# Performance work log

Hardware: AMD Instinct MI355X
Metric: run time of the kernel (lower is better)

The kernel has to match this reference:

```python
import jax, jax.numpy as jnp
import numpy as np

DIM = 384
HEADS = 12
HEAD_DIM = DIM // HEADS
WIN = (2, 7, 7)
NW_TOK = WIN[0] * WIN[1] * WIN[2]  # 98
SCALE = HEAD_DIM ** -0.5


def _relative_position_index():
    d = np.arange(WIN[0]); h = np.arange(WIN[1]); w = np.arange(WIN[2])
    coords = np.stack(np.meshgrid(d, h, w, indexing='ij'))  # [3,D,H,W]
    cf = coords.reshape(3, -1)  # [3, NW_TOK]
    rel = cf[:, :, None] - cf[:, None, :]  # [3, N, N]
    rel = rel.transpose(1, 2, 0).astype(np.int64)
    rel[:, :, 0] += WIN[0] - 1
    rel[:, :, 1] += WIN[1] - 1
    rel[:, :, 2] += WIN[2] - 1
    rel[:, :, 0] *= (2 * WIN[1] - 1) * (2 * WIN[2] - 1)
    rel[:, :, 1] *= 2 * WIN[2] - 1
    return rel.sum(-1)  # [NW_TOK, NW_TOK]


def setup_inputs() -> dict:
    key = jax.random.key(0)
    ks = jax.random.split(key, 6)
    B_, N = 1024, NW_TOK + 1
    nW = 64
    table_len = (2 * WIN[0] - 1) * (2 * WIN[1] - 1) * (2 * WIN[2] - 1)  # 507
    x = jax.random.normal(ks[0], (B_, N, DIM), dtype=jnp.float32)
    mask = jax.random.normal(ks[1], (nW, NW_TOK, NW_TOK), dtype=jnp.float32)
    W_qkv = jax.random.normal(ks[2], (DIM, 3 * DIM), dtype=jnp.float32) * 0.02
    rpb_table = jax.random.normal(ks[3], (table_len, HEADS), dtype=jnp.float32) * 0.02
    W_proj = jax.random.normal(ks[4], (DIM, DIM), dtype=jnp.float32) * 0.02
    b_proj = jnp.zeros((DIM,), dtype=jnp.float32)
    rpi = jnp.asarray(_relative_position_index(), dtype=jnp.int32)
    return {"x": x, "mask": mask, "W_qkv": W_qkv, "rpb_table": rpb_table,
            "W_proj": W_proj, "b_proj": b_proj, "rpi": rpi}


def reference(x, mask, W_qkv, rpb_table, W_proj, b_proj, rpi):
    B_, N, C = x.shape
    qkv = (x @ W_qkv).reshape(B_, N, 3, HEADS, HEAD_DIM)
    q, k, v = qkv[:, :, 0], qkv[:, :, 1], qkv[:, :, 2]  # [B_, N, H, hd]
    attn = jnp.einsum('bnhd,bmhd->bhnm', q * SCALE, k)  # [B_, H, N, N]
    # gathered relative position bias over non-class tokens, zero-padded for class token
    bias = rpb_table[rpi.reshape(-1)].reshape(NW_TOK, NW_TOK, HEADS).transpose(2, 0, 1)
    bias_full = jnp.pad(bias, ((0, 0), (1, 0), (1, 0)))  # [H, N, N]
    attn = attn + bias_full[None]
    nW = mask.shape[0]
    mask_full = jnp.pad(mask, ((0, 0), (1, 0), (1, 0)))  # [nW, N, N]
    attn = attn.reshape(B_ // nW, nW, HEADS, N, N) + mask_full[None, :, None]
    attn = attn.reshape(B_, HEADS, N, N)
    attn = jax.nn.softmax(attn, axis=-1)
    out = jnp.einsum('bhnm,bmhd->bnhd', attn, v).reshape(B_, N, C)
    out = out @ W_proj + b_proj
    return out[:, 1:], out[:, :1]
```

## Files before the change

kernel.cpp:

```cpp
#include <hip/hip_runtime.h>
#include <hip/hip_bf16.h>
#include <cstddef>
#include <cstdint>


using bf16 = __hip_bfloat16;
typedef short v8s __attribute__((ext_vector_type(8)));
typedef short v4s __attribute__((ext_vector_type(4)));
typedef float v4f __attribute__((ext_vector_type(4)));

static constexpr int    NTOK   = 99;
static constexpr int    CDIM   = 384;
static constexpr int    NHEAD  = 12;
static constexpr int    NROWS  = 101376;
static constexpr size_t PLANE  = (size_t)NROWS * 32;
static constexpr float  SCALEF = 0.17677669529663687f;

__device__ __forceinline__ v4f mfma16x16x32(v8s a, v8s b, v4f c) {
  return __builtin_amdgcn_mfma_f32_16x16x32_bf16(a, b, c, 0, 0, 0);
}
__device__ __forceinline__ short f2bf(float f) {
  bf16 h = __float2bfloat16(f);
  return *reinterpret_cast<short*>(&h);
}
__device__ __forceinline__ float bf2f(short s) {
  bf16 h = *reinterpret_cast<bf16*>(&s);
  return __bfloat162float(h);
}

#if defined(__has_builtin)
#if __has_builtin(__builtin_amdgcn_global_load_lds)
#define HAS_GLL 1
#endif
#endif
#ifndef HAS_GLL
#define HAS_GLL 0
#endif

__device__ __forceinline__ void gload_lds16(const bf16* gsrc, bf16* ldst, int lane) {
#if HAS_GLL
  __builtin_amdgcn_global_load_lds(
      (const __attribute__((address_space(1))) void*)gsrc,
      (__attribute__((address_space(3))) void*)ldst, 16, 0, 0);
#else
  *(v8s*)(ldst + lane * 8) = *(const v8s*)gsrc;
#endif
}

static constexpr size_t WT_QKV_OFF = 0;
static constexpr size_t WT_P_OFF   = 884736;
static constexpr size_t BIAS_OFF   = 884736 + 294912;
static constexpr size_t COMMON_END = 1650096;
static constexpr size_t O_WS_OFF   = COMMON_END;
static constexpr size_t WS_MID     = O_WS_OFF + (size_t)NROWS * 384 * 2;
static constexpr size_t BMF_OFF    = COMMON_END;
static constexpr size_t BMF_BYTES  = (size_t)64 * NHEAD * 7 * 7 * 64 * 4 * 2;
static constexpr size_t QKV_OFF    = BMF_OFF + BMF_BYTES;
static constexpr size_t WS_FULL    = QKV_OFF + (size_t)NROWS * 1152 * 2;

static constexpr int PREP_BASE = 1152 * 384 + 384 * 384 + NHEAD * 99 * 99;
static constexpr int PREP_BMF2 = 64 * 112 * 112;

__global__ void prep_kernel(const float* __restrict__ Wqkv, const float* __restrict__ Wproj,
                            const float* __restrict__ rpb,  const int* __restrict__ rpi,
                            const float* __restrict__ mask,
                            bf16* __restrict__ WtQKV, bf16* __restrict__ WtP,
                            float* __restrict__ BIAS, bf16* __restrict__ BMF, int do_bmf)
{
  int idx = blockIdx.x * 256 + threadIdx.x;
  if (idx < 1152 * 384) {
    int c = idx / 384, k = idx - c * 384;
    WtQKV[idx] = __float2bfloat16(Wqkv[k * 1152 + c]);
  } else if (idx < 1152 * 384 + 384 * 384) {
    int j = idx - 1152 * 384;
    int c = j / 384, k = j - c * 384;
    WtP[j] = __float2bfloat16(Wproj[k * 384 + c]);
  } else if (idx < PREP_BASE) {
    int j = idx - (1152 * 384 + 384 * 384);
    int h = j / (99 * 99), r = j % (99 * 99);
    int nn = r / 99, mm = r % 99;
    float v = 0.f;
    if (nn > 0 && mm > 0) v = rpb[rpi[(nn - 1) * 98 + (mm - 1)] * NHEAD + h];
    BIAS[j] = v;
  } else if (do_bmf && idx < PREP_BASE + PREP_BMF2) {
    int j2  = idx - PREP_BASE;
    int col = j2 % 112;
    int r2  = j2 / 112;
    int row = r2 % 112;
    int wi  = r2 / 112;
    int w = row >> 4, g = (row >> 2) & 3, jj = row & 3;
    int t = col >> 4, li = col & 15, lane = g * 16 + li;
    bool in = (row >= 1 && row <= 98 && col >= 1 && col <= 98);
    int tix = 0; float mval = 0.f;
    if (in) {
      tix  = rpi[(row - 1) * 98 + (col - 1)];
      mval = mask[((size_t)wi * 98 + (row - 1)) * 98 + (col - 1)];
    }
    size_t base = (((size_t)wi * NHEAD * 7 + w) * 7 + t) * 256 + lane * 4 + jj;
    #pragma unroll
    for (int h = 0; h < NHEAD; ++h) {
      float v = in ? (rpb[tix * NHEAD + h] + mval) : 0.f;
      BMF[base + (size_t)h * 12544] = __float2bfloat16(v);
    }
  }
}

static constexpr int GQB_OFF  = 0;
static constexpr int GQA_OFF  = 24576;
static constexpr int GQ_LDS2  = GQA_OFF + 128 * 72 * 2;
static constexpr int CSTG_LD  = 104;

__global__ __launch_bounds__(512)
void k_qkv(const float* __restrict__ x, const bf16* __restrict__ WtQKV,
           bf16* __restrict__ qkv2)
{
  __shared__ __align__(16) char smem[GQ_LDS2];
  bf16* B_lds = (bf16*)(smem + GQB_OFF);
  bf16* A_lds = (bf16*)(smem + GQA_OFF);
  bf16* C_stg = (bf16*)(smem);

  const int tid  = threadIdx.x;
  const int wave = tid >> 6;
  const int wm   = wave >> 2;
  const int wn   = wave & 3;
  const int lane = tid & 63;
  const int g    = lane >> 4;
  const int li   = lane & 15;
  const int tile = (blockIdx.x & 7) * 594 + (blockIdx.x >> 3);
  const int R0   = (tile / 6) * 128;
  const int CN   = (tile % 6) * 192;

  const int arr = tid >> 3, ak8 = tid & 7;

  v4f acc[4][3];
  #pragma unroll
  for (int mi = 0; mi < 4; ++mi)
    #pragma unroll
    for (int ni = 0; ni < 3; ++ni) acc[mi][ni] = (v4f){0.f, 0.f, 0.f, 0.f};

  v4f areg[2][2];
  auto load_areg = [&](int kc) {
    const int k0 = kc * 64;
    #pragma unroll
    for (int p = 0; p < 2; ++p) {
      const float* src = x + (size_t)(R0 + arr + p * 64) * 384 + k0 + ak8 * 8;
      areg[p][0] = *(const v4f*)(src);
      areg[p][1] = *(const v4f*)(src + 4);
    }
  };
  auto write_alds = [&]() {
    #pragma unroll
    for (int p = 0; p < 2; ++p) {
      v8s f;
      #pragma unroll
      for (int j = 0; j < 4; ++j) { f[j] = f2bf(areg[p][0][j]); f[j + 4] = f2bf(areg[p][1][j]); }
      *(v8s*)(A_lds + (arr + p * 64) * 72 + ak8 * 8) = f;
    }
  };

  load_areg(0);

  for (int kc = 0; kc < 6; ++kc) {
    const int k0 = kc * 64;
    write_alds();
    #pragma unroll
    for (int p = 0; p < 3; ++p) {
      int q   = wave * 3 + p;
      int row = q * 8 + (lane >> 3);
      int c   = (lane & 7) ^ (row & 7);
      const bf16* gsrc = WtQKV + (size_t)(CN + row) * 384 + k0 + c * 8;
      gload_lds16(gsrc, B_lds + q * 512, lane);
    }
    if (kc < 5) load_areg(kc + 1);
    __syncthreads();
    #pragma unroll
    for (int ks = 0; ks < 2; ++ks) {
      v8s af[4], bfr[3];
      #pragma unroll
      for (int mi = 0; mi < 4; ++mi)
        af[mi] = *(const v8s*)(A_lds + (wm * 64 + mi * 16 + li) * 72 + ks * 32 + g * 8);
      #pragma unroll
      for (int ni = 0; ni < 3; ++ni) {
        int brow = wn * 48 + ni * 16 + li;
        int sc   = (g + 4 * ks) ^ (brow & 7);
        bfr[ni]  = *(const v8s*)(B_lds + brow * 64 + sc * 8);
      }
      #pragma unroll
      for (int mi = 0; mi < 4; ++mi)
        #pragma unroll
        for (int ni = 0; ni < 3; ++ni)
          acc[mi][ni] = mfma16x16x32(af[mi], bfr[ni], acc[mi][ni]);
    }
    __syncthreads();
  }

  const float scale = (CN < 384) ? SCALEF : 1.f;
  const int r_ep = tid >> 2, d8 = tid & 3;
  #pragma unroll
  for (int half = 0; half < 2; ++half) {
    __syncthreads();
    if ((wn >> 1) == half) {
      #pragma unroll
      for (int mi = 0; mi < 4; ++mi)
        #pragma unroll
        for (int ni = 0; ni < 3; ++ni)
          #pragma unroll
          for (int j = 0; j < 4; ++j)
            C_stg[(wm * 64 + mi * 16 + g * 4 + j) * CSTG_LD + (wn & 1) * 48 + ni * 16 + li] =
                __float2bfloat16(acc[mi][ni][j] * scale);
    }
    __syncthreads();
    #pragma unroll
    for (int cidx = 0; cidx < 3; ++cidx) {
      int c_global = CN + half * 96 + cidx * 32;
      int seg = c_global / 384, hh = (c_global % 384) >> 5;
      bf16* plane = qkv2 + (size_t)(hh * 3 + seg) * PLANE;
      v8s val = *(const v8s*)(C_stg + r_ep * CSTG_LD + cidx * 32 + d8 * 8);
      *(v8s*)(plane + (size_t)(R0 + r_ep) * 32 + d8 * 8) = val;
    }
  }
}

static constexpr int A_VT_LD = 136;
static constexpr int A_P_LD  = 136;
static constexpr int A_OFF_V = 0;
static constexpr int A_OFF_P = A_OFF_V + 32 * A_VT_LD * 2;
static constexpr int A_LDS   = A_OFF_P + 112 * A_P_LD * 2;

__global__ __launch_bounds__(448)
void k_attn(const bf16* __restrict__ BMF, bf16* __restrict__ qkv2)
{
  __shared__ __align__(16) char smem[A_LDS];
  bf16* vT_lds = (bf16*)(smem + A_OFF_V);
  bf16* P_lds  = (bf16*)(smem + A_OFF_P);

  const int b    = blockIdx.x;
  const int h0   = blockIdx.y * 3;
  const int tid  = threadIdx.x;
  const int wave = tid >> 6;
  const int lane = tid & 63;
  const int g    = lane >> 4;
  const int li   = lane & 15;
  const int wi   = b & 63;

  for (int z = tid; z < 32 * 29; z += 448)
    vT_lds[(z / 29) * A_VT_LD + 99 + (z % 29)] = __float2bfloat16(0.f);
  for (int z = tid; z < 112 * 29; z += 448)
    P_lds[(z / 29) * A_P_LD + 99 + (z % 29)] = __float2bfloat16(0.f);

  const int r = tid >> 2, l4 = tid & 3;
  const size_t voff = ((size_t)b * NTOK + ((r > 98) ? 98 : r)) * 32 + l4 * 8;

  const int qrow = (16 * wave + li > 98) ? 98 : 16 * wave + li;
  const size_t qoff = ((size_t)b * NTOK + qrow) * 32 + g * 8;
  size_t koff[7];
  #pragma unroll
  for (int t = 0; t < 7; ++t) {
    int krow = 16 * t + li; if (krow > 98) krow = 98;
    koff[t] = ((size_t)b * NTOK + krow) * 32 + g * 8;
  }

  {
    v8s pv = *(const v8s*)(qkv2 + (size_t)(h0 * 3 + 2) * PLANE + voff);
    if (r < NTOK) {
      #pragma unroll
      for (int e = 0; e < 8; ++e)
        *(short*)(vT_lds + (l4 * 8 + e) * A_VT_LD + r) = pv[e];
    }
  }
  __syncthreads();

  v4f oaccs[3][2];

  #pragma unroll
  for (int hi = 0; hi < 3; ++hi) {
    const int h = h0 + hi;
    v8s nv;
    if (hi < 2) nv = *(const v8s*)(qkv2 + (size_t)(h * 3 + 5) * PLANE + voff);

    const bf16* kp = qkv2 + (size_t)(h * 3 + 1) * PLANE;
    v8s kf[7];
    #pragma unroll
    for (int t = 0; t < 7; ++t) kf[t] = *(const v8s*)(kp + koff[t]);
    v8s qf = *(const v8s*)(qkv2 + (size_t)(h * 3 + 0) * PLANE + qoff);

    const bf16* bmb = BMF + ((size_t)((wi * NHEAD + h) * 7 + wave) * 7) * 256;
    v4s bmr[7];
    #pragma unroll
    for (int t = 0; t < 7; ++t)
      bmr[t] = *(const v4s*)(bmb + t * 256 + lane * 4);

    v4f sacc[7];
    #pragma unroll
    for (int t = 0; t < 7; ++t) {
      v4f z = (v4f){0.f, 0.f, 0.f, 0.f};
      sacc[t] = mfma16x16x32(qf, kf[t], z);
    }
    #pragma unroll
    for (int t = 0; t < 7; ++t) {
      int col = 16 * t + li;
      #pragma unroll
      for (int j = 0; j < 4; ++j) {
        float s = sacc[t][j];
        if (col >= NTOK) s = -1e30f;
        else             s += bf2f(bmr[t][j]);
        sacc[t][j] = s;
      }
    }
    float linv[4];
    #pragma unroll
    for (int j = 0; j < 4; ++j) {
      float m = -1e30f;
      #pragma unroll
      for (int t = 0; t < 7; ++t) m = fmaxf(m, sacc[t][j]);
      m = fmaxf(m, __shfl_xor(m, 1));
      m = fmaxf(m, __shfl_xor(m, 2));
      m = fmaxf(m, __shfl_xor(m, 4));
      m = fmaxf(m, __shfl_xor(m, 8));
      float l = 0.f;
      #pragma unroll
      for (int t = 0; t < 7; ++t) {
        float p = __expf(sacc[t][j] - m);
        sacc[t][j] = p;
        l += p;
      }
      l += __shfl_xor(l, 1);
      l += __shfl_xor(l, 2);
      l += __shfl_xor(l, 4);
      l += __shfl_xor(l, 8);
      linv[j] = 1.f / l;
      int row = 16 * wave + g * 4 + j;
      #pragma unroll
      for (int t = 0; t < 7; ++t) {
        int col = 16 * t + li;
        if (col < NTOK) P_lds[row * A_P_LD + col] = __float2bfloat16(sacc[t][j]);
      }
    }
    v4f oacc[2];
    oacc[0] = (v4f){0.f, 0.f, 0.f, 0.f};
    oacc[1] = (v4f){0.f, 0.f, 0.f, 0.f};
    #pragma unroll
    for (int ks = 0; ks < 4; ++ks) {
      v8s ap = *(const v8s*)(P_lds + (16 * wave + li) * A_P_LD + ks * 32 + g * 8);
      #pragma unroll
      for (int t = 0; t < 2; ++t) {
        v8s bv = *(const v8s*)(vT_lds + (16 * t + li) * A_VT_LD + ks * 32 + g * 8);
        oacc[t] = mfma16x16x32(ap, bv, oacc[t]);
      }
    }
    #pragma unroll
    for (int t = 0; t < 2; ++t)
      #pragma unroll
      for (int j = 0; j < 4; ++j)
        oaccs[hi][t][j] = oacc[t][j] * linv[j];

    __syncthreads();
    if (hi < 2) {
      if (r < NTOK) {
        #pragma unroll
        for (int e = 0; e < 8; ++e)
          *(short*)(vT_lds + (l4 * 8 + e) * A_VT_LD + r) = nv[e];
      }
      __syncthreads();
    }
  }

  #pragma unroll
  for (int hi = 0; hi < 3; ++hi) {
    bf16* oplane = qkv2 + (size_t)((h0 + hi) * 3) * PLANE;
    #pragma unroll
    for (int t = 0; t < 2; ++t)
      #pragma unroll
      for (int j = 0; j < 4; ++j) {
        int row = 16 * wave + g * 4 + j;
        if (row < NTOK)
          oplane[((size_t)b * NTOK + row) * 32 + 16 * t + li] =
              __float2bfloat16(oaccs[hi][t][j]);
      }
  }
}

static constexpr int K2_LD   = 72;
static constexpr int K2_OFFW = 0;
static constexpr int K2_OFFO = 192 * K2_LD * 2;
static constexpr int K2_LDS  = K2_OFFO + 128 * K2_LD * 2;

__global__ __launch_bounds__(512)
void k2_proj(const bf16* __restrict__ O_src, const int hm,
             const bf16* __restrict__ WtP, const float* __restrict__ bproj,
             float* __restrict__ out)
{
  __shared__ __align__(16) char smem[K2_LDS];
  bf16* W_lds = (bf16*)(smem + K2_OFFW);
  bf16* O_lds = (bf16*)(smem + K2_OFFO);

  const int tid  = threadIdx.x;
  const int wave = tid >> 6;
  const int wm   = wave >> 2;
  const int wn   = wave & 3;
  const int lane = tid & 63;
  const int g    = lane >> 4;
  const int li   = lane & 15;
  const int tile = (blockIdx.x & 7) * 198 + (blockIdx.x >> 3);
  const int R0   = (tile >> 1) * 128;
  const int CN   = (tile & 1) * 192;

  v4f acc[4][3];
  #pragma unroll
  for (int mi = 0; mi < 4; ++mi)
    #pragma unroll
    for (int ni = 0; ni < 3; ++ni) acc[mi][ni] = (v4f){0.f, 0.f, 0.f, 0.f};

  for (int kc = 0; kc < 6; ++kc) {
    const int k0 = kc * 64;
    #pragma unroll
    for (int p = 0; p < 3; ++p) {
      int it = tid + p * 512, rr = it >> 3, k8 = it & 7;
      *(v8s*)(W_lds + rr * K2_LD + k8 * 8) =
          *(const v8s*)(WtP + (size_t)(CN + rr) * CDIM + k0 + k8 * 8);
    }
    #pragma unroll
    for (int p = 0; p < 2; ++p) {
      int it = tid + p * 512, rr = it >> 3, k8 = it & 7;
      const bf16* src;
      if (hm) {
        int c = k0 + k8 * 8, hh = c >> 5, d = c & 31;
        src = O_src + (size_t)(hh * 3) * PLANE + (size_t)(R0 + rr) * 32 + d;
      } else {
        src = O_src + (size_t)(R0 + rr) * 384 + k0 + k8 * 8;
      }
      *(v8s*)(O_lds + rr * K2_LD + k8 * 8) = *(const v8s*)src;
    }
    __syncthreads();
    #pragma unroll
    for (int ks = 0; ks < 2; ++ks) {
      v8s af[4], bfr[3];
      #pragma unroll
      for (int mi = 0; mi < 4; ++mi)
        af[mi] = *(const v8s*)(O_lds + (wm * 64 + mi * 16 + li) * K2_LD + ks * 32 + g * 8);
      #pragma unroll
      for (int ni = 0; ni < 3; ++ni)
        bfr[ni] = *(const v8s*)(W_lds + (wn * 48 + ni * 16 + li) * K2_LD + ks * 32 + g * 8);
      #pragma unroll
      for (int mi = 0; mi < 4; ++mi)
        #pragma unroll
        for (int ni = 0; ni < 3; ++ni)
          acc[mi][ni] = mfma16x16x32(af[mi], bfr[ni], acc[mi][ni]);
    }
    __syncthreads();
  }

  const size_t OUT2 = (size_t)1024 * 98 * CDIM;
  #pragma unroll
  for (int mi = 0; mi < 4; ++mi)
    #pragma unroll
    for (int ni = 0; ni < 3; ++ni) {
      int col = CN + wn * 48 + ni * 16 + li;
      float bb = bproj[col];
      #pragma unroll
      for (int j = 0; j < 4; ++j) {
        int rr = R0 + wm * 64 + mi * 16 + g * 4 + j;
        int b = rr / 99, n = rr - b * 99;
        float v = acc[mi][ni][j] + bb;
        if (n == 0) out[OUT2 + (size_t)b * CDIM + col] = v;
        else        out[((size_t)b * 98 + (n - 1)) * CDIM + col] = v;
      }
    }
}

static constexpr int QK_LD = 40;
static constexpr int VT_LD = 136;
static constexpr int P_LD  = 136;
static constexpr int WS_LD = 104;
static constexpr int K1_OFF_Q = 0;
static constexpr int K1_OFF_K = K1_OFF_Q + 112 * QK_LD * 2;
static constexpr int K1_OFF_V = K1_OFF_K + 112 * QK_LD * 2;
static constexpr int K1_OFF_P = K1_OFF_V + 32  * VT_LD * 2;
static constexpr int K1_OFF_W = K1_OFF_P + 112 * P_LD  * 2;
static constexpr int K1_LDS   = K1_OFF_W + 96 * WS_LD * 2;

__global__ __launch_bounds__(512)
void k1_attn(const float* __restrict__ x, const float* __restrict__ mask,
             const float* __restrict__ BIAS, const bf16* __restrict__ WtQKV,
             bf16* __restrict__ O_ws)
{
  __shared__ __align__(16) char smem[K1_LDS];
  bf16* q_lds  = (bf16*)(smem + K1_OFF_Q);
  bf16* k_lds  = (bf16*)(smem + K1_OFF_K);
  bf16* vT_lds = (bf16*)(smem + K1_OFF_V);
  bf16* P_lds  = (bf16*)(smem + K1_OFF_P);
  bf16* w_lds  = (bf16*)(smem + K1_OFF_W);

  const int b    = blockIdx.x;
  const int tid  = threadIdx.x;
  const int wave = tid >> 6;
  const int lane = tid & 63;
  const int g    = lane >> 4;
  const int li   = lane & 15;
  const int wi   = b & 63;

  v8s afr[12];
  if (wave < 7) {
    int arow = 16 * wave + li; if (arow > 98) arow = 98;
    const float* xb = x + ((size_t)b * NTOK + arow) * CDIM + g * 8;
    #pragma unroll
    for (int s = 0; s < 12; ++s) {
      v4f x0 = *(const v4f*)(xb + s * 32);
      v4f x1 = *(const v4f*)(xb + s * 32 + 4);
      v8s f;
      #pragma unroll
      for (int j = 0; j < 4; ++j) { f[j] = f2bf(x0[j]); f[j + 4] = f2bf(x1[j]); }
      afr[s] = f;
    }
  }

  for (int h = 0; h < NHEAD; ++h) {
    v4f qacc[6];
    #pragma unroll
    for (int t = 0; t < 6; ++t) qacc[t] = (v4f){0.f, 0.f, 0.f, 0.f};
    #pragma unroll
    for (int c4 = 0; c4 < 4; ++c4) {
      for (int idx = tid; idx < 96 * 12; idx += 512) {
        int rr = idx / 12, ch = idx - rr * 12;
        int cg = (rr < 32) ? (h * 32 + rr)
               : (rr < 64) ? (CDIM + h * 32 + rr - 32)
                           : (2 * CDIM + h * 32 + rr - 64);
        *(v8s*)(w_lds + rr * WS_LD + ch * 8) =
            *(const v8s*)(WtQKV + (size_t)cg * CDIM + c4 * 96 + ch * 8);
      }
      __syncthreads();
      if (wave < 7) {
        #pragma unroll
        for (int ss = 0; ss < 3; ++ss) {
          const int s = c4 * 3 + ss;
          #pragma unroll
          for (int t = 0; t < 6; ++t) {
            v8s bw = *(const v8s*)(w_lds + (16 * t + li) * WS_LD + ss * 32 + g * 8);
            qacc[t] = mfma16x16x32(afr[s], bw, qacc[t]);
          }
        }
      }
      __syncthreads();
    }
    if (wave < 7) {
      #pragma unroll
      for (int t = 0; t < 6; ++t) {
        #pragma unroll
        for (int j = 0; j < 4; ++j) {
          int row = 16 * wave + g * 4 + j;
          int col = 16 * (t & 1) + li;
          float v = qacc[t][j];
          if (t < 2)      q_lds[row * QK_LD + col] = __float2bfloat16(v * SCALEF);
          else if (t < 4) k_lds[row * QK_LD + col] = __float2bfloat16(v);
          else            vT_lds[col * VT_LD + row] = __float2bfloat16(v);
        }
      }
    }
    vT_lds[(tid >> 4) * VT_LD + 112 + (tid & 15)] = __float2bfloat16(0.f);
    __syncthreads();

    if (wave < 7) {
      v8s aq = *(const v8s*)(q_lds + (16 * wave + li) * QK_LD + g * 8);
      v4f sacc[7];
      #pragma unroll
      for (int t = 0; t < 7; ++t) {
        v8s bk = *(const v8s*)(k_lds + (16 * t + li) * QK_LD + g * 8);
        v4f z = (v4f){0.f, 0.f, 0.f, 0.f};
        sacc[t] = mfma16x16x32(aq, bk, z);
      }
      #pragma unroll
      for (int t = 0; t < 7; ++t) {
        int col = 16 * t + li;
        #pragma unroll
        for (int j = 0; j < 4; ++j) {
          int row = 16 * wave + g * 4 + j;
          float s = sacc[t][j];
          if (col >= NTOK) s = -1e30f;
          else if (row < NTOK) {
            s += BIAS[(h * NTOK + row) * NTOK + col];
            if (row > 0 && col > 0)
              s += mask[((size_t)wi * 98 + (row - 1)) * 98 + (col - 1)];
          }
          sacc[t][j] = s;
        }
      }
      float linv[4];
      #pragma unroll
      for (int j = 0; j < 4; ++j) {
        float m = -1e30f;
        #pragma unroll
        for (int t = 0; t < 7; ++t) m = fmaxf(m, sacc[t][j]);
        m = fmaxf(m, __shfl_xor(m, 1));
        m = fmaxf(m, __shfl_xor(m, 2));
        m = fmaxf(m, __shfl_xor(m, 4));
        m = fmaxf(m, __shfl_xor(m, 8));
        float l = 0.f;
        #pragma unroll
        for (int t = 0; t < 7; ++t) {
          float p = __expf(sacc[t][j] - m);
          sacc[t][j] = p;
          l += p;
        }
        l += __shfl_xor(l, 1);
        l += __shfl_xor(l, 2);
        l += __shfl_xor(l, 4);
        l += __shfl_xor(l, 8);
        linv[j] = 1.f / l;
        int row = 16 * wave + g * 4 + j;
        #pragma unroll
        for (int t = 0; t < 7; ++t)
          P_lds[row * P_LD + 16 * t + li] = __float2bfloat16(sacc[t][j]);
        P_lds[row * P_LD + 112 + li] = __float2bfloat16(0.f);
      }
      v4f oacc[2];
      oacc[0] = (v4f){0.f, 0.f, 0.f, 0.f};
      oacc[1] = (v4f){0.f, 0.f, 0.f, 0.f};
      #pragma unroll
      for (int ks = 0; ks < 4; ++ks) {
        v8s ap = *(const v8s*)(P_lds + (16 * wave + li) * P_LD + ks * 32 + g * 8);
        #pragma unroll
        for (int t = 0; t < 2; ++t) {
          v8s bv = *(const v8s*)(vT_lds + (16 * t + li) * VT_LD + ks * 32 + g * 8);
          oacc[t] = mfma16x16x32(ap, bv, oacc[t]);
        }
      }
      #pragma unroll
      for (int t = 0; t < 2; ++t) {
        #pragma unroll
        for (int j = 0; j < 4; ++j) {
          int row = 16 * wave + g * 4 + j;
          if (row < NTOK)
            O_ws[((size_t)b * 99 + row) * CDIM + h * 32 + 16 * t + li] =
                __float2bfloat16(oacc[t][j] * linv[j]);
        }
      }
    }
    __syncthreads();
  }
}

static constexpr int M_O_LD = 392;
static constexpr int M_OFF_O = 0;
static constexpr int M_OFF_Q = M_OFF_O + 99  * M_O_LD * 2;
static constexpr int M_OFF_K = M_OFF_Q + 112 * QK_LD * 2;
static constexpr int M_OFF_V = M_OFF_K + 112 * QK_LD * 2;
static constexpr int M_OFF_P = M_OFF_V + 32  * VT_LD * 2;
static constexpr int M_OFF_W = M_OFF_P + 112 * P_LD  * 2;
static constexpr int M_LDS   = M_OFF_W + 96 * WS_LD * 2;

__global__ __launch_bounds__(512)
void fused_mono(const float* __restrict__ x, const float* __restrict__ mask,
                const float* __restrict__ bproj, const float* __restrict__ BIAS,
                const bf16* __restrict__ WtQKV, const bf16* __restrict__ WtP,
                float* __restrict__ out)
{
  __shared__ __align__(16) char smem[M_LDS];
  bf16* O_lds  = (bf16*)(smem + M_OFF_O);
  bf16* q_lds  = (bf16*)(smem + M_OFF_Q);
  bf16* k_lds  = (bf16*)(smem + M_OFF_K);
  bf16* vT_lds = (bf16*)(smem + M_OFF_V);
  bf16* P_lds  = (bf16*)(smem + M_OFF_P);
  bf16* w_lds  = (bf16*)(smem + M_OFF_W);

  const int b    = blockIdx.x;
  const int tid  = threadIdx.x;
  const int wave = tid >> 6;
  const int lane = tid & 63;
  const int g    = lane >> 4;
  const int li   = lane & 15;
  const int wi   = b & 63;

  v8s afr[12];
  if (wave < 7) {
    int arow = 16 * wave + li; if (arow > 98) arow = 98;
    const float* xb = x + ((size_t)b * NTOK + arow) * CDIM + g * 8;
    #pragma unroll
    for (int s = 0; s < 12; ++s) {
      v4f x0 = *(const v4f*)(xb + s * 32);
      v4f x1 = *(const v4f*)(xb + s * 32 + 4);
      v8s f;
      #pragma unroll
      for (int j = 0; j < 4; ++j) { f[j] = f2bf(x0[j]); f[j + 4] = f2bf(x1[j]); }
      afr[s] = f;
    }
  }

  for (int h = 0; h < NHEAD; ++h) {
    v4f qacc[6];
    #pragma unroll
    for (int t = 0; t < 6; ++t) qacc[t] = (v4f){0.f, 0.f, 0.f, 0.f};
    #pragma unroll
    for (int c4 = 0; c4 < 4; ++c4) {
      for (int idx = tid; idx < 96 * 12; idx += 512) {
        int rr = idx / 12, ch = idx - rr * 12;
        int cg = (rr < 32) ? (h * 32 + rr)
               : (rr < 64) ? (CDIM + h * 32 + rr - 32)
                           : (2 * CDIM + h * 32 + rr - 64);
        *(v8s*)(w_lds + rr * WS_LD + ch * 8) =
            *(const v8s*)(WtQKV + (size_t)cg * CDIM + c4 * 96 + ch * 8);
      }
      __syncthreads();
      if (wave < 7) {
        #pragma unroll
        for (int ss = 0; ss < 3; ++ss) {
          const int s = c4 * 3 + ss;
          #pragma unroll
          for (int t = 0; t < 6; ++t) {
            v8s bw = *(const v8s*)(w_lds + (16 * t + li) * WS_LD + ss * 32 + g * 8);
            qacc[t] = mfma16x16x32(afr[s], bw, qacc[t]);
          }
        }
      }
      __syncthreads();
    }
    if (wave < 7) {
      #pragma unroll
      for (int t = 0; t < 6; ++t) {
        #pragma unroll
        for (int j = 0; j < 4; ++j) {
          int row = 16 * wave + g * 4 + j;
          int col = 16 * (t & 1) + li;
          float v = qacc[t][j];
          if (t < 2)      q_lds[row * QK_LD + col] = __float2bfloat16(v * SCALEF);
          else if (t < 4) k_lds[row * QK_LD + col] = __float2bfloat16(v);
          else            vT_lds[col * VT_LD + row] = __float2bfloat16(v);
        }
      }
    }
    vT_lds[(tid >> 4) * VT_LD + 112 + (tid & 15)] = __float2bfloat16(0.f);
    __syncthreads();

    if (wave < 7) {
      v8s aq = *(const v8s*)(q_lds + (16 * wave + li) * QK_LD + g * 8);
      v4f sacc[7];
      #pragma unroll
      for (int t = 0; t < 7; ++t) {
        v8s bk = *(const v8s*)(k_lds + (16 * t + li) * QK_LD + g * 8);
        v4f z = (v4f){0.f, 0.f, 0.f, 0.f};
        sacc[t] = mfma16x16x32(aq, bk, z);
      }
      #pragma unroll
      for (int t = 0; t < 7; ++t) {
        int col = 16 * t + li;
        #pragma unroll
        for (int j = 0; j < 4; ++j) {
          int row = 16 * wave + g * 4 + j;
          float s = sacc[t][j];
          if (col >= NTOK) s = -1e30f;
          else if (row < NTOK) {
            s += BIAS[(h * NTOK + row) * NTOK + col];
            if (row > 0 && col > 0)
              s += mask[((size_t)wi * 98 + (row - 1)) * 98 + (col - 1)];
          }
          sacc[t][j] = s;
        }
      }
      float linv[4];
      #pragma unroll
      for (int j = 0; j < 4; ++j) {
        float m = -1e30f;
        #pragma unroll
        for (int t = 0; t < 7; ++t) m = fmaxf(m, sacc[t][j]);
        m = fmaxf(m, __shfl_xor(m, 1));
        m = fmaxf(m, __shfl_xor(m, 2));
        m = fmaxf(m, __shfl_xor(m, 4));
        m = fmaxf(m, __shfl_xor(m, 8));
        float l = 0.f;
        #pragma unroll
        for (int t = 0; t < 7; ++t) {
          float p = __expf(sacc[t][j] - m);
          sacc[t][j] = p;
          l += p;
        }
        l += __shfl_xor(l, 1);
        l += __shfl_xor(l, 2);
        l += __shfl_xor(l, 4);
        l += __shfl_xor(l, 8);
        linv[j] = 1.f / l;
        int row = 16 * wave + g * 4 + j;
        #pragma unroll
        for (int t = 0; t < 7; ++t)
          P_lds[row * P_LD + 16 * t + li] = __float2bfloat16(sacc[t][j]);
        P_lds[row * P_LD + 112 + li] = __float2bfloat16(0.f);
      }
      v4f oacc[2];
      oacc[0] = (v4f){0.f, 0.f, 0.f, 0.f};
      oacc[1] = (v4f){0.f, 0.f, 0.f, 0.f};
      #pragma unroll
      for (int ks = 0; ks < 4; ++ks) {
        v8s ap = *(const v8s*)(P_lds + (16 * wave + li) * P_LD + ks * 32 + g * 8);
        #pragma unroll
        for (int t = 0; t < 2; ++t) {
          v8s bv = *(const v8s*)(vT_lds + (16 * t + li) * VT_LD + ks * 32 + g * 8);
          oacc[t] = mfma16x16x32(ap, bv, oacc[t]);
        }
      }
      #pragma unroll
      for (int t = 0; t < 2; ++t) {
        #pragma unroll
        for (int j = 0; j < 4; ++j) {
          int row = 16 * wave + g * 4 + j;
          if (row < NTOK)
            O_lds[row * M_O_LD + h * 32 + 16 * t + li] =
                __float2bfloat16(oacc[t][j] * linv[j]);
        }
      }
    }
    __syncthreads();
  }

  const size_t OUT2 = (size_t)1024 * 98 * CDIM;
  const int orow_clamped = (16 * wave + li > 98) ? 98 : 16 * wave + li;
  for (int cc = 0; cc < 4; ++cc) {
    v4f pacc[6];
    #pragma unroll
    for (int t = 0; t < 6; ++t) pacc[t] = (v4f){0.f, 0.f, 0.f, 0.f};
    for (int c4 = 0; c4 < 4; ++c4) {
      for (int idx = tid; idx < 96 * 12; idx += 512) {
        int rr = idx / 12, ch = idx - rr * 12;
        *(v8s*)(w_lds + rr * WS_LD + ch * 8) =
            *(const v8s*)(WtP + ((size_t)(cc * 96 + rr)) * CDIM + c4 * 96 + ch * 8);
      }
      __syncthreads();
      if (wave < 7) {
        #pragma unroll
        for (int ss = 0; ss < 3; ++ss) {
          const int s = c4 * 3 + ss;
          v8s ao = *(const v8s*)(O_lds + orow_clamped * M_O_LD + s * 32 + g * 8);
          #pragma unroll
          for (int t = 0; t < 6; ++t) {
            v8s bw = *(const v8s*)(w_lds + (16 * t + li) * WS_LD + ss * 32 + g * 8);
            pacc[t] = mfma16x16x32(ao, bw, pacc[t]);
          }
        }
      }
      __syncthreads();
    }
    if (wave < 7) {
      #pragma unroll
      for (int t = 0; t < 6; ++t) {
        #pragma unroll
        for (int j = 0; j < 4; ++j) {
          int row = 16 * wave + g * 4 + j;
          if (row < NTOK) {
            int col = cc * 96 + 16 * t + li;
            float v = pacc[t][j] + bproj[col];
            if (row == 0) out[OUT2 + (size_t)b * CDIM + col] = v;
            else          out[((size_t)b * 98 + (row - 1)) * CDIM + col] = v;
          }
        }
      }
    }
  }
}

extern "C" void kernel_launch(void* const* d_in, const int* in_sizes, int n_in,
                              void* d_out, int out_size, void* d_ws, size_t ws_size,
                              hipStream_t stream) {
  const float* x     = (const float*)d_in[0];
  const float* mask  = (const float*)d_in[1];
  const float* Wqkv  = (const float*)d_in[2];
  const float* rpb   = (const float*)d_in[3];
  const float* Wproj = (const float*)d_in[4];
  const float* bproj = (const float*)d_in[5];
  const int*   rpi   = (const int*)d_in[6];

  bf16*  WtQKV = (bf16*)((char*)d_ws + WT_QKV_OFF);
  bf16*  WtP   = (bf16*)((char*)d_ws + WT_P_OFF);
  float* BIAS  = (float*)((char*)d_ws + BIAS_OFF);
  bf16*  BMF   = (bf16*)((char*)d_ws + BMF_OFF);

  const bool full = (ws_size >= WS_FULL);
  const int prep_items = full ? (PREP_BASE + PREP_BMF2) : PREP_BASE;
  prep_kernel<<<(prep_items + 255) / 256, 256, 0, stream>>>(
      Wqkv, Wproj, rpb, rpi, mask, WtQKV, WtP, BIAS, BMF, full ? 1 : 0);

  if (full) {
    bf16* qkv2 = (bf16*)((char*)d_ws + QKV_OFF);
    k_qkv<<<792 * 6, 512, 0, stream>>>(x, WtQKV, qkv2);
    k_attn<<<dim3(1024, 4), 448, 0, stream>>>(BMF, qkv2);
    k2_proj<<<792 * 2, 512, 0, stream>>>(qkv2, 1, WtP, bproj, (float*)d_out);
  } else if (ws_size >= WS_MID) {
    bf16* O_ws = (bf16*)((char*)d_ws + O_WS_OFF);
    k1_attn<<<1024, 512, 0, stream>>>(x, mask, BIAS, WtQKV, O_ws);
    k2_proj<<<792 * 2, 512, 0, stream>>>(O_ws, 0, WtP, bproj, (float*)d_out);
  } else {
    fused_mono<<<1024, 512, 0, stream>>>(x, mask, bproj, BIAS, WtQKV, WtP,
                                         (float*)d_out);
  }
}
```

Measured before the change: 434.1 us.

## Pre-convert x to bf16 and double-buffer QKV/proj GEMMs with direct LDS loads

Adds a pass in the prep kernel that converts x to bf16 into a new workspace buffer. New k_qkv2 and k2_proj2 kernels stage A and B tiles with global_load_lds into double-buffered, XOR-swizzled LDS and use vmcnt waits, so loads overlap the MFMA work. The goal is to hide global-load latency, avoid LDS bank conflicts and drop the fp32-to-bf16 conversion from the GEMM inner loop. In exchange it costs extra workspace plus an additional read and write pass over x, and the new path is taken only when the workspace is large enough.

```diff
diff --git a/kernel.cpp b/kernel.cpp
--- a/kernel.cpp
+++ b/kernel.cpp
@@ -57,15 +57,19 @@
 static constexpr size_t BMF_BYTES  = (size_t)64 * NHEAD * 7 * 7 * 64 * 4 * 2;
 static constexpr size_t QKV_OFF    = BMF_OFF + BMF_BYTES;
 static constexpr size_t WS_FULL    = QKV_OFF + (size_t)NROWS * 1152 * 2;
+static constexpr size_t XB_OFF     = WS_FULL;
+static constexpr size_t WS_FULL2   = XB_OFF + (size_t)NROWS * 384 * 2;
 
 static constexpr int PREP_BASE = 1152 * 384 + 384 * 384 + NHEAD * 99 * 99;
 static constexpr int PREP_BMF2 = 64 * 112 * 112;
+static constexpr int PREP_XB   = NROWS * 384 / 8;
 
 __global__ void prep_kernel(const float* __restrict__ Wqkv, const float* __restrict__ Wproj,
                             const float* __restrict__ rpb,  const int* __restrict__ rpi,
-                            const float* __restrict__ mask,
+                            const float* __restrict__ mask, const float* __restrict__ x,
                             bf16* __restrict__ WtQKV, bf16* __restrict__ WtP,
-                            float* __restrict__ BIAS, bf16* __restrict__ BMF, int do_bmf)
+                            float* __restrict__ BIAS, bf16* __restrict__ BMF,
+                            bf16* __restrict__ xb, int do_bmf, int do_xb)
 {
   int idx = blockIdx.x * 256 + threadIdx.x;
   if (idx < 1152 * 384) {
@@ -102,21 +106,28 @@
       float v = in ? (rpb[tix * NHEAD + h] + mval) : 0.f;
       BMF[base + (size_t)h * 12544] = __float2bfloat16(v);
     }
-  }
-}
-
-static constexpr int GQB_OFF  = 0;
-static constexpr int GQA_OFF  = 24576;
-static constexpr int GQ_LDS2  = GQA_OFF + 128 * 72 * 2;
-static constexpr int CSTG_LD  = 104;
+  } else if (do_xb && idx >= PREP_BASE + PREP_BMF2 &&
+             idx < PREP_BASE + PREP_BMF2 + PREP_XB) {
+    int j3 = idx - (PREP_BASE + PREP_BMF2);
+    size_t off = (size_t)j3 * 8;
+    v4f x0 = *(const v4f*)(x + off);
+    v4f x1 = *(const v4f*)(x + off + 4);
+    v8s f;
+    #pragma unroll
+    for (int j = 0; j < 4; ++j) { f[j] = f2bf(x0[j]); f[j + 4] = f2bf(x1[j]); }
+    *(v8s*)(xb + off) = f;
+  }
+}
+
+static constexpr int Q2_BUF  = 40960;
+static constexpr int Q2_AOFF = 24576;
+static constexpr int CSTG_LD = 104;
 
 __global__ __launch_bounds__(512)
-void k_qkv(const float* __restrict__ x, const bf16* __restrict__ WtQKV,
-           bf16* __restrict__ qkv2)
+void k_qkv2(const bf16* __restrict__ xb, const bf16* __restrict__ WtQKV,
+            bf16* __restrict__ qkv2)
 {
-  __shared__ __align__(16) char smem[GQ_LDS2];
-  bf16* B_lds = (bf16*)(smem + GQB_OFF);
-  bf16* A_lds = (bf16*)(smem + GQA_OFF);
+  __shared__ __align__(16) char smem[2 * Q2_BUF];
   bf16* C_stg = (bf16*)(smem);
 
   const int tid  = threadIdx.x;
@@ -130,6 +141,120 @@
   const int R0   = (tile / 6) * 128;
   const int CN   = (tile % 6) * 192;
 
+  v4f acc[4][3];
+  #pragma unroll
+  for (int mi = 0; mi < 4; ++mi)
+    #pragma unroll
+    for (int ni = 0; ni < 3; ++ni) acc[mi][ni] = (v4f){0.f, 0.f, 0.f, 0.f};
+
+  auto stage = [&](int kc, int buf) {
+    const int k0 = kc * 64;
+    bf16* Bl = (bf16*)(smem + buf * Q2_BUF);
+    bf16* Al = (bf16*)(smem + buf * Q2_BUF + Q2_AOFF);
+    #pragma unroll
+    for (int p = 0; p < 3; ++p) {
+      int q = wave * 3 + p;
+      int row = q * 8 + (lane >> 3);
+      int c = (lane & 7) ^ (row & 7);
+      gload_lds16(WtQKV + (size_t)(CN + row) * 384 + k0 + c * 8, Bl + q * 512, lane);
+    }
+    #pragma unroll
+    for (int p = 0; p < 2; ++p) {
+      int q = wave * 2 + p;
+      int row = q * 8 + (lane >> 3);
+      int c = (lane & 7) ^ (row & 7);
+      gload_lds16(xb + (size_t)(R0 + row) * 384 + k0 + c * 8, Al + q * 512, lane);
+    }
+  };
+
+  stage(0, 0);
+  for (int kc = 0; kc < 6; ++kc) {
+    if (kc < 5) {
+      stage(kc + 1, (kc + 1) & 1);
+      asm volatile("s_waitcnt vmcnt(5)" ::: "memory");
+    } else {
+      asm volatile("s_waitcnt vmcnt(0)" ::: "memory");
+    }
+    __builtin_amdgcn_s_barrier();
+    __builtin_amdgcn_sched_barrier(0);
+    const bf16* Bl = (const bf16*)(smem + (kc & 1) * Q2_BUF);
+    const bf16* Al = (const bf16*)(smem + (kc & 1) * Q2_BUF + Q2_AOFF);
+    #pragma unroll
+    for (int ks = 0; ks < 2; ++ks) {
+      v8s af[4], bfr[3];
+      #pragma unroll
+      for (int mi = 0; mi < 4; ++mi) {
+        int arow = wm * 64 + mi * 16 + li;
+        int sc   = (4 * ks + g) ^ (arow & 7);
+        af[mi] = *(const v8s*)(Al + arow * 64 + sc * 8);
+      }
+      #pragma unroll
+      for (int ni = 0; ni < 3; ++ni) {
+        int brow = wn * 48 + ni * 16 + li;
+        int sc   = (4 * ks + g) ^ (brow & 7);
+        bfr[ni] = *(const v8s*)(Bl + brow * 64 + sc * 8);
+      }
+      #pragma unroll
+      for (int mi = 0; mi < 4; ++mi)
+        #pragma unroll
+        for (int ni = 0; ni < 3; ++ni)
+          acc[mi][ni] = mfma16x16x32(af[mi], bfr[ni], acc[mi][ni]);
+    }
+    __builtin_amdgcn_sched_barrier(0);
+    __builtin_amdgcn_s_barrier();
+  }
+
+  const float scale = (CN < 384) ? SCALEF : 1.f;
+  const int r_ep = tid >> 2, d8 = tid & 3;
+  #pragma unroll
+  for (int half = 0; half < 2; ++half) {
+    __syncthreads();
+    if ((wn >> 1) == half) {
+      #pragma unroll
+      for (int mi = 0; mi < 4; ++mi)
+        #pragma unroll
+        for (int ni = 0; ni < 3; ++ni)
+          #pragma unroll
+          for (int j = 0; j < 4; ++j)
+            C_stg[(wm * 64 + mi * 16 + g * 4 + j) * CSTG_LD + (wn & 1) * 48 + ni * 16 + li] =
+                __float2bfloat16(acc[mi][ni][j] * scale);
+    }
+    __syncthreads();
+    #pragma unroll
+    for (int cidx = 0; cidx < 3; ++cidx) {
+      int c_global = CN + half * 96 + cidx * 32;
+      int seg = c_global / 384, hh = (c_global % 384) >> 5;
+      bf16* plane = qkv2 + (size_t)(hh * 3 + seg) * PLANE;
+      v8s val = *(const v8s*)(C_stg + r_ep * CSTG_LD + cidx * 32 + d8 * 8);
+      *(v8s*)(plane + (size_t)(R0 + r_ep) * 32 + d8 * 8) = val;
+    }
+  }
+}
+
+static constexpr int GQB_OFF  = 0;
+static constexpr int GQA_OFF  = 24576;
+static constexpr int GQ_LDS2  = GQA_OFF + 128 * 72 * 2;
+
+__global__ __launch_bounds__(512)
+void k_qkv(const float* __restrict__ x, const bf16* __restrict__ WtQKV,
+           bf16* __restrict__ qkv2)
+{
+  __shared__ __align__(16) char smem[GQ_LDS2];
+  bf16* B_lds = (bf16*)(smem + GQB_OFF);
+  bf16* A_lds = (bf16*)(smem + GQA_OFF);
+  bf16* C_stg = (bf16*)(smem);
+
+  const int tid  = threadIdx.x;
+  const int wave = tid >> 6;
+  const int wm   = wave >> 2;
+  const int wn   = wave & 3;
+  const int lane = tid & 63;
+  const int g    = lane >> 4;
+  const int li   = lane & 15;
+  const int tile = (blockIdx.x & 7) * 594 + (blockIdx.x >> 3);
+  const int R0   = (tile / 6) * 128;
+  const int CN   = (tile % 6) * 192;
+
   const int arr = tid >> 3, ak8 = tid & 7;
 
   v4f acc[4][3];
@@ -380,19 +505,11 @@
   }
 }
 
-static constexpr int K2_LD   = 72;
-static constexpr int K2_OFFW = 0;
-static constexpr int K2_OFFO = 192 * K2_LD * 2;
-static constexpr int K2_LDS  = K2_OFFO + 128 * K2_LD * 2;
-
 __global__ __launch_bounds__(512)
-void k2_proj(const bf16* __restrict__ O_src, const int hm,
-             const bf16* __restrict__ WtP, const float* __restrict__ bproj,
-             float* __restrict__ out)
+void k2_proj2(const bf16* __restrict__ O_src, const bf16* __restrict__ WtP,
+              const float* __restrict__ bproj, float* __restrict__ out)
 {
-  __shared__ __align__(16) char smem[K2_LDS];
-  bf16* W_lds = (bf16*)(smem + K2_OFFW);
-  bf16* O_lds = (bf16*)(smem + K2_OFFO);
+  __shared__ __align__(16) char smem[2 * Q2_BUF];
 
   const int tid  = threadIdx.x;
   const int wave = tid >> 6;
@@ -411,6 +528,113 @@
     #pragma unroll
     for (int ni = 0; ni < 3; ++ni) acc[mi][ni] = (v4f){0.f, 0.f, 0.f, 0.f};
 
+  auto stage = [&](int kc, int buf) {
+    const int k0 = kc * 64;
+    bf16* Wl = (bf16*)(smem + buf * Q2_BUF);
+    bf16* Ol = (bf16*)(smem + buf * Q2_BUF + Q2_AOFF);
+    #pragma unroll
+    for (int p = 0; p < 3; ++p) {
+      int q = wave * 3 + p;
+      int row = q * 8 + (lane >> 3);
+      int c = (lane & 7) ^ (row & 7);
+      gload_lds16(WtP + (size_t)(CN + row) * CDIM + k0 + c * 8, Wl + q * 512, lane);
+    }
+    #pragma unroll
+    for (int p = 0; p < 2; ++p) {
+      int q = wave * 2 + p;
+      int row = q * 8 + (lane >> 3);
+      int c = (lane & 7) ^ (row & 7);
+      int kk = k0 + c * 8, hh = kk >> 5, d = kk & 31;
+      gload_lds16(O_src + (size_t)(hh * 3) * PLANE + (size_t)(R0 + row) * 32 + d,
+                  Ol + q * 512, lane);
+    }
+  };
+
+  stage(0, 0);
+  for (int kc = 0; kc < 6; ++kc) {
+    if (kc < 5) {
+      stage(kc + 1, (kc + 1) & 1);
+      asm volatile("s_waitcnt vmcnt(5)" ::: "memory");
+    } else {
+      asm volatile("s_waitcnt vmcnt(0)" ::: "memory");
+    }
+    __builtin_amdgcn_s_barrier();
+    __builtin_amdgcn_sched_barrier(0);
+    const bf16* Wl = (const bf16*)(smem + (kc & 1) * Q2_BUF);
+    const bf16* Ol = (const bf16*)(smem + (kc & 1) * Q2_BUF + Q2_AOFF);
+    #pragma unroll
+    for (int ks = 0; ks < 2; ++ks) {
+      v8s af[4], bfr[3];
+      #pragma unroll
+      for (int mi = 0; mi < 4; ++mi) {
+        int arow = wm * 64 + mi * 16 + li;
+        int sc   = (4 * ks + g) ^ (arow & 7);
+        af[mi] = *(const v8s*)(Ol + arow * 64 + sc * 8);
+      }
+      #pragma unroll
+      for (int ni = 0; ni < 3; ++ni) {
+        int brow = wn * 48 + ni * 16 + li;
+        int sc   = (4 * ks + g) ^ (brow & 7);
+        bfr[ni] = *(const v8s*)(Wl + brow * 64 + sc * 8);
+      }
+      #pragma unroll
+      for (int mi = 0; mi < 4; ++mi)
+        #pragma unroll
+        for (int ni = 0; ni < 3; ++ni)
+          acc[mi][ni] = mfma16x16x32(af[mi], bfr[ni], acc[mi][ni]);
+    }
+    __builtin_amdgcn_sched_barrier(0);
+    __builtin_amdgcn_s_barrier();
+  }
+
+  const size_t OUT2 = (size_t)1024 * 98 * CDIM;
+  #pragma unroll
+  for (int mi = 0; mi < 4; ++mi)
+    #pragma unroll
+    for (int ni = 0; ni < 3; ++ni) {
+      int col = CN + wn * 48 + ni * 16 + li;
+      float bb = bproj[col];
+      #pragma unroll
+      for (int j = 0; j < 4; ++j) {
+        int rr = R0 + wm * 64 + mi * 16 + g * 4 + j;
+        int b = rr / 99, n = rr - b * 99;
+        float v = acc[mi][ni][j] + bb;
+        if (n == 0) out[OUT2 + (size_t)b * CDIM + col] = v;
+        else        out[((size_t)b * 98 + (n - 1)) * CDIM + col] = v;
+      }
+    }
+}
+
+static constexpr int K2_LD   = 72;
+static constexpr int K2_OFFW = 0;
+static constexpr int K2_OFFO = 192 * K2_LD * 2;
+static constexpr int K2_LDS  = K2_OFFO + 128 * K2_LD * 2;
+
+__global__ __launch_bounds__(512)
+void k2_proj(const bf16* __restrict__ O_src, const bf16* __restrict__ WtP,
+             const float* __restrict__ bproj, float* __restrict__ out)
+{
+  __shared__ __align__(16) char smem[K2_LDS];
+  bf16* W_lds = (bf16*)(smem + K2_OFFW);
+  bf16* O_lds = (bf16*)(smem + K2_OFFO);
+
+  const int tid  = threadIdx.x;
+  const int wave = tid >> 6;
+  const int wm   = wave >> 2;
+  const int wn   = wave & 3;
+  const int lane = tid & 63;
+  const int g    = lane >> 4;
+  const int li   = lane & 15;
+  const int tile = (blockIdx.x & 7) * 198 + (blockIdx.x >> 3);
+  const int R0   = (tile >> 1) * 128;
+  const int CN   = (tile & 1) * 192;
+
+  v4f acc[4][3];
+  #pragma unroll
+  for (int mi = 0; mi < 4; ++mi)
+    #pragma unroll
+    for (int ni = 0; ni < 3; ++ni) acc[mi][ni] = (v4f){0.f, 0.f, 0.f, 0.f};
+
   for (int kc = 0; kc < 6; ++kc) {
     const int k0 = kc * 64;
     #pragma unroll
@@ -422,14 +646,8 @@
     #pragma unroll
     for (int p = 0; p < 2; ++p) {
       int it = tid + p * 512, rr = it >> 3, k8 = it & 7;
-      const bf16* src;
-      if (hm) {
-        int c = k0 + k8 * 8, hh = c >> 5, d = c & 31;
-        src = O_src + (size_t)(hh * 3) * PLANE + (size_t)(R0 + rr) * 32 + d;
-      } else {
-        src = O_src + (size_t)(R0 + rr) * 384 + k0 + k8 * 8;
-      }
-      *(v8s*)(O_lds + rr * K2_LD + k8 * 8) = *(const v8s*)src;
+      *(v8s*)(O_lds + rr * K2_LD + k8 * 8) =
+          *(const v8s*)(O_src + (size_t)(R0 + rr) * 384 + k0 + k8 * 8);
     }
     __syncthreads();
     #pragma unroll
@@ -869,21 +1087,27 @@
   bf16*  WtP   = (bf16*)((char*)d_ws + WT_P_OFF);
   float* BIAS  = (float*)((char*)d_ws + BIAS_OFF);
   bf16*  BMF   = (bf16*)((char*)d_ws + BMF_OFF);
-
-  const bool full = (ws_size >= WS_FULL);
-  const int prep_items = full ? (PREP_BASE + PREP_BMF2) : PREP_BASE;
+  bf16*  xbuf  = (bf16*)((char*)d_ws + XB_OFF);
+
+  const bool full2 = (ws_size >= WS_FULL2);
+  const bool full  = (ws_size >= WS_FULL);
+  int prep_items = PREP_BASE;
+  if (full)  prep_items += PREP_BMF2;
+  if (full2) prep_items += PREP_XB;
   prep_kernel<<<(prep_items + 255) / 256, 256, 0, stream>>>(
-      Wqkv, Wproj, rpb, rpi, mask, WtQKV, WtP, BIAS, BMF, full ? 1 : 0);
+      Wqkv, Wproj, rpb, rpi, mask, x, WtQKV, WtP, BIAS, BMF, xbuf,
+      full ? 1 : 0, full2 ? 1 : 0);
 
   if (full) {
     bf16* qkv2 = (bf16*)((char*)d_ws + QKV_OFF);
-    k_qkv<<<792 * 6, 512, 0, stream>>>(x, WtQKV, qkv2);
+    if (full2) k_qkv2<<<792 * 6, 512, 0, stream>>>(xbuf, WtQKV, qkv2);
+    else       k_qkv<<<792 * 6, 512, 0, stream>>>(x, WtQKV, qkv2);
     k_attn<<<dim3(1024, 4), 448, 0, stream>>>(BMF, qkv2);
-    k2_proj<<<792 * 2, 512, 0, stream>>>(qkv2, 1, WtP, bproj, (float*)d_out);
+    k2_proj2<<<792 * 2, 512, 0, stream>>>(qkv2, WtP, bproj, (float*)d_out);
   } else if (ws_size >= WS_MID) {
     bf16* O_ws = (bf16*)((char*)d_ws + O_WS_OFF);
     k1_attn<<<1024, 512, 0, stream>>>(x, mask, BIAS, WtQKV, O_ws);
-    k2_proj<<<792 * 2, 512, 0, stream>>>(O_ws, 0, WtP, bproj, (float*)d_out);
+    k2_proj<<<792 * 2, 512, 0, stream>>>(O_ws, WtP, bproj, (float*)d_out);
   } else {
     fused_mono<<<1024, 512, 0, stream>>>(x, mask, bproj, BIAS, WtQKV, WtP,
                                          (float*)d_out);
```

Result: no change. 442.3 us (+1.9%).
